# Kernel optimization log

Hardware: AMD Instinct MI355X
Metric: run time of the kernel (lower is better)

## Reference

```python
import jax, jax.numpy as jnp
import numpy as np

LN_EPS = 1e-9

def _layer_norm(x, g, b):
    mu = jnp.mean(x, axis=-1, keepdims=True)
    var = jnp.mean((x - mu) ** 2, axis=-1, keepdims=True)
    return (x - mu) * jax.lax.rsqrt(var + LN_EPS) * g + b

def _ffn(x, w1, b1, w2, b2, ln_g, ln_b):
    h = jax.nn.gelu(x @ w1 + b1, approximate=False)
    h = h @ w2 + b2
    return _layer_norm(h, ln_g, ln_b)

def _kernel_mean(x, y):
    d = x.shape[1]
    x2 = jnp.sum(x * x, axis=1)[:, None]
    y2 = jnp.sum(y * y, axis=1)[None, :]
    sq = x2 + y2 - 2.0 * (x @ y.T)  # [Nx, Ny]
    return jnp.mean(jnp.exp(-sq / (d * d)))

def _mmd(x, y):
    return _kernel_mean(x, x) + _kernel_mean(y, y) - 2.0 * _kernel_mean(x, y)

def setup_inputs() -> dict:
    key = jax.random.key(0)
    ks = jax.random.split(key, 8)
    B, S, D, DI, DL = 8, 512, 1024, 4096, 64
    s = lambda fan: 1.0 / np.sqrt(fan)
    return {
        "hidden": jax.random.normal(ks[0], (B, S, D), jnp.float32),
        "true_samples": jax.random.normal(ks[1], (B * S, DL), jnp.float32),
        "enc_w1": jax.random.normal(ks[2], (D, DI), jnp.float32) * s(D),
        "enc_b1": jnp.zeros((DI,), jnp.float32),
        "enc_w2": jax.random.normal(ks[3], (DI, DL), jnp.float32) * s(DI),
        "enc_b2": jnp.zeros((DL,), jnp.float32),
        "enc_ln_g": jnp.ones((DL,), jnp.float32),
        "enc_ln_b": jnp.zeros((DL,), jnp.float32),
        "dec_w1": jax.random.normal(ks[4], (DL, DI), jnp.float32) * s(DL),
        "dec_b1": jnp.zeros((DI,), jnp.float32),
        "dec_w2": jax.random.normal(ks[5], (DI, D), jnp.float32) * s(DI),
        "dec_b2": jnp.zeros((D,), jnp.float32),
        "dec_ln_g": jnp.ones((D,), jnp.float32),
        "dec_ln_b": jnp.zeros((D,), jnp.float32),
    }

def reference(hidden, true_samples, enc_w1, enc_b1, enc_w2, enc_b2, enc_ln_g, enc_ln_b,
              dec_w1, dec_b1, dec_w2, dec_b2, dec_ln_g, dec_ln_b):
    latent = _ffn(hidden, enc_w1, enc_b1, enc_w2, enc_b2, enc_ln_g, enc_ln_b)  # [B,S,DL]
    recon = _ffn(latent, dec_w1, dec_b1, dec_w2, dec_b2, dec_ln_g, dec_ln_b)   # [B,S,D]
    B, S, DL = latent.shape
    lat_flat = latent.reshape(-1, DL)  # [B*S, DL]
    reg_loss = _mmd(true_samples, lat_flat) / B * S
    return recon, latent, reg_loss
```

## Files before the change

### kernel.cpp

```cpp
#include <hip/hip_runtime.h>
#include <hip/hip_bf16.h>
#include <math.h>


typedef __attribute__((ext_vector_type(8))) short short8;
typedef __attribute__((ext_vector_type(4))) float float4a;
typedef __attribute__((ext_vector_type(4))) unsigned short us4;

__device__ inline ushort bf16r(float x) {
    union { float f; unsigned u; } c; c.f = x;
    unsigned r = (c.u + 0x7fffu + ((c.u >> 16) & 1u)) >> 16;
    return (ushort)r;
}

__device__ inline void gld_lds16(const void* g, void* l) {
    __builtin_amdgcn_global_load_lds(
        (const __attribute__((address_space(1))) void*)g,
        (__attribute__((address_space(3))) void*)l, 16, 0, 0);
}

template <int N> __device__ inline void wait_vmcnt() {
    if constexpr (N == 0) asm volatile("s_waitcnt vmcnt(0)" ::: "memory");
    else if constexpr (N == 4) asm volatile("s_waitcnt vmcnt(4)" ::: "memory");
    else if constexpr (N == 6) asm volatile("s_waitcnt vmcnt(6)" ::: "memory");
}

template <int N> __device__ inline void wait_lgkmcnt() {
    if constexpr (N == 0) asm volatile("s_waitcnt lgkmcnt(0)" ::: "memory");
    else if constexpr (N == 2) asm volatile("s_waitcnt lgkmcnt(2)" ::: "memory");
    else if constexpr (N == 4) asm volatile("s_waitcnt lgkmcnt(4)" ::: "memory");
    else if constexpr (N == 6) asm volatile("s_waitcnt lgkmcnt(6)" ::: "memory");
    else if constexpr (N == 8) asm volatile("s_waitcnt lgkmcnt(8)" ::: "memory");
    else if constexpr (N == 12) asm volatile("s_waitcnt lgkmcnt(12)" ::: "memory");
}

__device__ inline float fast_gelu(float v) {
    float v2 = v * v;
    float u = v * __builtin_fmaf(0.07135481627f, v2, 1.5957691216f);
    u = fminf(u, 30.0f);
    float e = __expf(u);
    return v * e * __builtin_amdgcn_rcpf(e + 1.0f);
}

__global__ __launch_bounds__(256) void k_pre(
        const float* __restrict__ hidden, ushort* __restrict__ A1bf,
        const float* __restrict__ tsamp, ushort* __restrict__ Tbf,
        float* __restrict__ sq_t, float* __restrict__ acc,
        const float* __restrict__ i0, ushort* __restrict__ o0,
        const float* __restrict__ i1, ushort* __restrict__ o1,
        const float* __restrict__ i2, ushort* __restrict__ o2,
        const float* __restrict__ i3, ushort* __restrict__ o3) {
    int b = blockIdx.x, tid = threadIdx.x;
    if (b == 0 && tid < 24) acc[tid] = 0.0f;
    if (b < 4096) {
        int i = b * 1024 + tid * 4;
        float4 v = *(const float4*)(hidden + i);
        us4 o = {bf16r(v.x), bf16r(v.y), bf16r(v.z), bf16r(v.w)};
        *(us4*)(A1bf + i) = o;
        return;
    }
    if (b < 4352) {
        int i = (b - 4096) * 1024 + tid * 4;
        float4 v = *(const float4*)(tsamp + i);
        us4 o = {bf16r(v.x), bf16r(v.y), bf16r(v.z), bf16r(v.w)};
        *(us4*)(Tbf + i) = o;
        float s = v.x * v.x + v.y * v.y + v.z * v.z + v.w * v.w;
#pragma unroll
        for (int off = 8; off; off >>= 1) s += __shfl_xor(s, off);
        if ((tid & 15) == 0) sq_t[i >> 6] = s;
        return;
    }
    __shared__ float t[32][65];
    const float* in; ushort* out; int R, C;
    int lb = b - 4352;
    if (lb < 2048)      { in = i0; out = o0; R = 1024; C = 4096; }
    else if (lb < 2176) { in = i1; out = o1; R = 4096; C = 64;   lb -= 2048; }
    else if (lb < 2304) { in = i2; out = o2; R = 64;   C = 4096; lb -= 2176; }
    else                { in = i3; out = o3; R = 4096; C = 1024; lb -= 2304; }
    int bx = (lb % (C / 32)) * 32;
    int by = (lb / (C / 32)) * 64;
    int tx = tid & 31, ty = tid >> 5;
#pragma unroll
    for (int i = 0; i < 64; i += 8)
        t[tx][i + ty] = in[(size_t)(by + i + ty) * C + (bx + tx)];
    __syncthreads();
#pragma unroll
    for (int i = 0; i < 32; i += 8) {
        int c = i + ty;
        ushort2 o;
        o.x = bf16r(t[c][2 * tx]);
        o.y = bf16r(t[c][2 * tx + 1]);
        *(ushort2*)(&out[(size_t)(bx + c) * R + by + 2 * tx]) = o;
    }
}

template <int BN, int EPI, bool SWZ>
__global__ __launch_bounds__(256) void k_gemm(
        const ushort* __restrict__ A, const ushort* __restrict__ Bt,
        const float* __restrict__ bias, void* __restrict__ Out,
        float* __restrict__ Out2, int M, int N, int K, int KC) {
    constexpr int BM = 128, BK = 64;
    constexpr int WAVES_N = BN / 64;
    constexpr int WAVES_M = 4 / WAVES_N;
    constexpr int WM = BM / WAVES_M;
    constexpr int MT = WM / 16;
    constexpr int NT = 4;
    constexpr int CA = BM / 32, CB = BN / 32;

    __shared__ ushort sA[BM * 64];
    __shared__ ushort sB[BN * 64];

    const int tid  = threadIdx.x;
    const int wave = tid >> 6, lane = tid & 63;
    const int wm = wave / WAVES_N, wn = wave % WAVES_N;
    int bx = blockIdx.x, by = blockIdx.y;
    if constexpr (SWZ) {
        int lin = blockIdx.x + gridDim.x * blockIdx.y;
        by = lin % gridDim.y;
        bx = lin / gridDim.y;
    }
    const int m0 = by * BM, n0 = bx * BN;
    const int lrow = lane & 15, lq = lane >> 4;
    const int srow8 = lane >> 3;
    const int sk8   = lane & 7;
    const int kbeg = blockIdx.z * KC;

    const ushort* pA[CA]; unsigned lA[CA];
#pragma unroll
    for (int j = 0; j < CA; ++j) {
        int c = wave * CA + j;
        int r = c * 8 + srow8;
        pA[j] = &A[(size_t)(m0 + r) * K + kbeg + ((sk8 ^ (r & 7)) * 8)];
        lA[j] = c * 512;
    }
    const ushort* pB[CB]; unsigned lB[CB];
#pragma unroll
    for (int j = 0; j < CB; ++j) {
        int c = wave * CB + j;
        int r = c * 8 + srow8;
        pB[j] = &Bt[(size_t)(n0 + r) * K + kbeg + ((sk8 ^ (r & 7)) * 8)];
        lB[j] = c * 512;
    }
    unsigned aoff[2][MT], boff[2][NT];
#pragma unroll
    for (int h = 0; h < 2; ++h) {
#pragma unroll
        for (int mt = 0; mt < MT; ++mt) {
            int r = wm * WM + mt * 16 + lrow;
            aoff[h][mt] = r * 64 + (((h * 4 + lq) ^ (r & 7)) * 8);
        }
#pragma unroll
        for (int nt = 0; nt < NT; ++nt) {
            int r = wn * 64 + nt * 16 + lrow;
            boff[h][nt] = r * 64 + (((h * 4 + lq) ^ (r & 7)) * 8);
        }
    }

    float4a acc[MT][NT];
#pragma unroll
    for (int mt = 0; mt < MT; ++mt)
#pragma unroll
        for (int nt = 0; nt < NT; ++nt)
            acc[mt][nt] = (float4a){0.f, 0.f, 0.f, 0.f};

    for (int k0 = 0; k0 < KC; k0 += BK) {
#pragma unroll
        for (int j = 0; j < CA; ++j) {
            gld_lds16(pA[j], &sA[lA[j]]);
            pA[j] += BK;
        }
#pragma unroll
        for (int j = 0; j < CB; ++j) {
            gld_lds16(pB[j], &sB[lB[j]]);
            pB[j] += BK;
        }
        __syncthreads();
#pragma unroll
        for (int h = 0; h < 2; ++h) {
            short8 af[MT], bfr[NT];
#pragma unroll
            for (int mt = 0; mt < MT; ++mt)
                af[mt] = *(short8*)(&sA[aoff[h][mt]]);
#pragma unroll
            for (int nt = 0; nt < NT; ++nt)
                bfr[nt] = *(short8*)(&sB[boff[h][nt]]);
#pragma unroll
            for (int mt = 0; mt < MT; ++mt)
#pragma unroll
                for (int nt = 0; nt < NT; ++nt)
                    acc[mt][nt] = __builtin_amdgcn_mfma_f32_16x16x32_bf16(
                        af[mt], bfr[nt], acc[mt][nt], 0, 0, 0);
        }
        __syncthreads();
    }

    float* dstp = nullptr;
    if constexpr (EPI == 2) {
        if (Out2 && blockIdx.z) dstp = Out2;
        else dstp = (float*)Out + (size_t)blockIdx.z * M * N;
    }
#pragma unroll
    for (int mt = 0; mt < MT; ++mt)
#pragma unroll
        for (int nt = 0; nt < NT; ++nt) {
            int col = n0 + wn * 64 + nt * 16 + lrow;
            float bv = 0.f;
            if constexpr (EPI != 2) bv = bias[col];
#pragma unroll
            for (int r = 0; r < 4; ++r) {
                int row = m0 + wm * WM + mt * 16 + lq * 4 + r;
                float v = acc[mt][nt][r] + bv;
                if constexpr (EPI == 0) {
                    ((ushort*)Out)[(size_t)row * N + col] = bf16r(fast_gelu(v));
                } else if constexpr (EPI == 1) {
                    ((float*)Out)[(size_t)row * N + col] = v;
                } else {
                    dstp[(size_t)row * N + col] = v;
                }
            }
        }
}

template <int BN, int EPI, int CX, int CY>
__global__ __launch_bounds__(512, 2) void k_gemm256mb(
        const ushort* __restrict__ A, const ushort* __restrict__ Bt,
        const float* __restrict__ bias, void* __restrict__ Out,
        float* __restrict__ Out2, int M, int N, int K, int KC) {
    constexpr int BM = 256, BK = 64;
    constexpr int AI = 4;
    constexpr int BI = BN / 64;
    constexpr int WAVES_N = BN / 64;
    constexpr int WAVES_M = 8 / WAVES_N;
    constexpr int WM = BM / WAVES_M;
    constexpr int MT = WM / 16;
    constexpr int NT = 4;

    __shared__ ushort sA[2][BM * 64];
    __shared__ ushort sB[2][BN * 64];

    const int tid = threadIdx.x;
    const int wave = tid >> 6, lane = tid & 63;
    const int wm = wave / WAVES_N, wn = wave % WAVES_N;

    const int gx = gridDim.x, gy = gridDim.y;
    const int lin = blockIdx.x + gx * (blockIdx.y + gy * blockIdx.z);
    const int nwg = gx * gy * gridDim.z;
    const int cpx = nwg >> 3;
    const int swz = (lin & 7) * cpx + (lin >> 3);
    const int nz  = gx * gy;
    const int zz  = swz / nz;
    const int rr  = swz % nz;
    const int chunk = rr / (CX * CY);
    const int lcl   = rr % (CX * CY);
    const int ncx   = gx / CX;
    const int bx = (chunk % ncx) * CX + (lcl % CX);
    const int by = (chunk / ncx) * CY + (lcl / CX);

    const int m0 = by * BM, n0 = bx * BN;
    const int lrow = lane & 15, lq = lane >> 4;
    const int kbeg = zz * KC;
    const int nT = KC / BK;

    const int crow = tid >> 3;
    const int ck8  = (tid & 7) ^ (crow & 7);
    const ushort* pAbase = A  + (size_t)(m0 + crow) * K + kbeg + ck8 * 8;
    const ushort* pBbase = Bt + (size_t)(n0 + crow) * K + kbeg + ck8 * 8;

    const int a0  = (wm * WM + lrow) * 64;
    const int b0  = (wn * 64 + lrow) * 64;
    const int sw0 = ((lq) ^ (lrow & 7)) * 8;
    const int sw1 = ((4 + lq) ^ (lrow & 7)) * 8;

    float4a acc[MT][NT];
#pragma unroll
    for (int mt = 0; mt < MT; ++mt)
#pragma unroll
        for (int nt = 0; nt < NT; ++nt)
            acc[mt][nt] = (float4a){0.f, 0.f, 0.f, 0.f};

#pragma unroll
    for (int j = 0; j < AI; ++j)
        gld_lds16(pAbase + (size_t)j * 64 * K, &sA[0][j * 4096 + wave * 512]);
#pragma unroll
    for (int j = 0; j < BI; ++j)
        gld_lds16(pBbase + (size_t)j * 64 * K, &sB[0][j * 4096 + wave * 512]);
    wait_vmcnt<0>();
    __builtin_amdgcn_s_barrier();
    __builtin_amdgcn_sched_barrier(0);

    for (int t = 0; t < nT; ++t) {
        const int d = t & 1;
        const bool pf1 = (t + 1 < nT);
        const size_t koff1 = (size_t)(t + 1) * BK;

        short8 af0[MT], bfr0[NT], af1[MT], bfr1[NT];
#pragma unroll
        for (int mt = 0; mt < MT; ++mt)
            af0[mt] = *(const short8*)(&sA[d][a0 + mt * 1024 + sw0]);
#pragma unroll
        for (int nt = 0; nt < NT; ++nt)
            bfr0[nt] = *(const short8*)(&sB[d][b0 + nt * 1024 + sw0]);
        __builtin_amdgcn_sched_barrier(0);
#pragma unroll
        for (int mt = 0; mt < MT; ++mt)
            af1[mt] = *(const short8*)(&sA[d][a0 + mt * 1024 + sw1]);
#pragma unroll
        for (int nt = 0; nt < NT; ++nt)
            bfr1[nt] = *(const short8*)(&sB[d][b0 + nt * 1024 + sw1]);
        if (pf1) {
#pragma unroll
            for (int j = 0; j < AI; ++j)
                gld_lds16(pAbase + (size_t)j * 64 * K + koff1,
                          &sA[d ^ 1][j * 4096 + wave * 512]);
#pragma unroll
            for (int j = 0; j < BI; ++j)
                gld_lds16(pBbase + (size_t)j * 64 * K + koff1,
                          &sB[d ^ 1][j * 4096 + wave * 512]);
        }
        wait_lgkmcnt<MT + 4>();
        __builtin_amdgcn_sched_barrier(0);
        __builtin_amdgcn_s_setprio(1);
#pragma unroll
        for (int mt = 0; mt < MT; ++mt)
#pragma unroll
            for (int nt = 0; nt < NT; ++nt)
                acc[mt][nt] = __builtin_amdgcn_mfma_f32_16x16x32_bf16(
                    af0[mt], bfr0[nt], acc[mt][nt], 0, 0, 0);
        __builtin_amdgcn_s_setprio(0);
        wait_lgkmcnt<0>();
        __builtin_amdgcn_sched_barrier(0);
        __builtin_amdgcn_s_setprio(1);
#pragma unroll
        for (int mt = 0; mt < MT; ++mt)
#pragma unroll
            for (int nt = 0; nt < NT; ++nt)
                acc[mt][nt] = __builtin_amdgcn_mfma_f32_16x16x32_bf16(
                    af1[mt], bfr1[nt], acc[mt][nt], 0, 0, 0);
        __builtin_amdgcn_s_setprio(0);
        if (pf1) {
            wait_vmcnt<0>();
            __builtin_amdgcn_s_barrier();
            __builtin_amdgcn_sched_barrier(0);
        }
    }

    float* dstp = nullptr;
    if constexpr (EPI == 2) {
        if (Out2 && zz) dstp = Out2;
        else dstp = (float*)Out + (size_t)zz * M * N;
    }
#pragma unroll
    for (int mt = 0; mt < MT; ++mt)
#pragma unroll
        for (int nt = 0; nt < NT; ++nt) {
            const int col = n0 + wn * 64 + nt * 16 + lrow;
            float bv = 0.f;
            if constexpr (EPI == 0) bv = bias[col];
#pragma unroll
            for (int r = 0; r < 4; ++r) {
                const int row = m0 + wm * WM + mt * 16 + lq * 4 + r;
                float v = acc[mt][nt][r] + bv;
                if constexpr (EPI == 0)
                    ((ushort*)Out)[(size_t)row * N + col] = bf16r(fast_gelu(v));
                else
                    dstp[(size_t)row * N + col] = v;
            }
        }
}

__global__ __launch_bounds__(512, 2) void k_gemm1f(
        const ushort* __restrict__ A, const ushort* __restrict__ Bt,
        const float* __restrict__ bias, const ushort* __restrict__ W2t,
        float* __restrict__ part, int M, int N, int K) {
    constexpr int BM = 256, BN = 256, BK = 64;
    constexpr int AI = 4, BI = 4;
    constexpr int WAVES_N = 4;
    constexpr int WM = 128;
    constexpr int MT = 8, NT = 4;
    constexpr int CX = 4, CY = 8;

    __shared__ ushort smem[65536];

    const int tid = threadIdx.x;
    const int wave = tid >> 6, lane = tid & 63;
    const int wm = wave / WAVES_N, wn = wave % WAVES_N;

    const int gx = gridDim.x, gy = gridDim.y;
    const int lin = blockIdx.x + gx * blockIdx.y;
    const int cpx = (gx * gy) >> 3;
    const int swz = (lin & 7) * cpx + (lin >> 3);
    const int chunk = swz / (CX * CY);
    const int lcl   = swz % (CX * CY);
    const int ncx   = gx / CX;
    const int bx = (chunk % ncx) * CX + (lcl % CX);
    const int by = (chunk / ncx) * CY + (lcl / CX);

    const int m0 = by * BM, n0 = bx * BN;
    const int lrow = lane & 15, lq = lane >> 4;
    const int nT = K / BK;

    const int crow = tid >> 3;
    const int ck8  = (tid & 7) ^ (crow & 7);
    const ushort* pAbase = A  + (size_t)(m0 + crow) * K + ck8 * 8;
    const ushort* pBbase = Bt + (size_t)(n0 + crow) * K + ck8 * 8;

    const int a0  = (wm * WM + lrow) * 64;
    const int b0  = (wn * 64 + lrow) * 64;
    const int sw0 = ((lq) ^ (lrow & 7)) * 8;
    const int sw1 = ((4 + lq) ^ (lrow & 7)) * 8;

    float4a acc[MT][NT];
#pragma unroll
    for (int mt = 0; mt < MT; ++mt)
#pragma unroll
        for (int nt = 0; nt < NT; ++nt)
            acc[mt][nt] = (float4a){0.f, 0.f, 0.f, 0.f};

#pragma unroll
    for (int j = 0; j < AI; ++j)
        gld_lds16(pAbase + (size_t)j * 64 * K, &smem[j * 4096 + wave * 512]);
#pragma unroll
    for (int j = 0; j < BI; ++j)
        gld_lds16(pBbase + (size_t)j * 64 * K,
                  &smem[32768 + j * 4096 + wave * 512]);
    wait_vmcnt<0>();
    __builtin_amdgcn_s_barrier();
    __builtin_amdgcn_sched_barrier(0);

    for (int t = 0; t < nT; ++t) {
        const int d = t & 1;
        const bool pf1 = (t + 1 < nT);
        const size_t koff1 = (size_t)(t + 1) * BK;
        const ushort* sAd = &smem[d * 16384];
        const ushort* sBd = &smem[32768 + d * 16384];

        short8 af0[MT], bfr0[NT], af1[MT], bfr1[NT];
#pragma unroll
        for (int mt = 0; mt < MT; ++mt)
            af0[mt] = *(const short8*)(&sAd[a0 + mt * 1024 + sw0]);
#pragma unroll
        for (int nt = 0; nt < NT; ++nt)
            bfr0[nt] = *(const short8*)(&sBd[b0 + nt * 1024 + sw0]);
        __builtin_amdgcn_sched_barrier(0);
#pragma unroll
        for (int mt = 0; mt < MT; ++mt)
            af1[mt] = *(const short8*)(&sAd[a0 + mt * 1024 + sw1]);
#pragma unroll
        for (int nt = 0; nt < NT; ++nt)
            bfr1[nt] = *(const short8*)(&sBd[b0 + nt * 1024 + sw1]);
        if (pf1) {
#pragma unroll
            for (int j = 0; j < AI; ++j)
                gld_lds16(pAbase + (size_t)j * 64 * K + koff1,
                          &smem[(d ^ 1) * 16384 + j * 4096 + wave * 512]);
#pragma unroll
            for (int j = 0; j < BI; ++j)
                gld_lds16(pBbase + (size_t)j * 64 * K + koff1,
                          &smem[32768 + (d ^ 1) * 16384 + j * 4096 + wave * 512]);
        }
        wait_lgkmcnt<12>();
        __builtin_amdgcn_sched_barrier(0);
        __builtin_amdgcn_s_setprio(1);
#pragma unroll
        for (int mt = 0; mt < MT; ++mt)
#pragma unroll
            for (int nt = 0; nt < NT; ++nt)
                acc[mt][nt] = __builtin_amdgcn_mfma_f32_16x16x32_bf16(
                    af0[mt], bfr0[nt], acc[mt][nt], 0, 0, 0);
        __builtin_amdgcn_s_setprio(0);
        wait_lgkmcnt<0>();
        __builtin_amdgcn_sched_barrier(0);
        __builtin_amdgcn_s_setprio(1);
#pragma unroll
        for (int mt = 0; mt < MT; ++mt)
#pragma unroll
            for (int nt = 0; nt < NT; ++nt)
                acc[mt][nt] = __builtin_amdgcn_mfma_f32_16x16x32_bf16(
                    af1[mt], bfr1[nt], acc[mt][nt], 0, 0, 0);
        __builtin_amdgcn_s_setprio(0);
        if (pf1) {
            wait_vmcnt<0>();
            __builtin_amdgcn_s_barrier();
            __builtin_amdgcn_sched_barrier(0);
        }
    }

    __syncthreads();
#pragma unroll
    for (int mt = 0; mt < MT; ++mt)
#pragma unroll
        for (int nt = 0; nt < NT; ++nt) {
            const int c = wn * 64 + nt * 16 + lrow;
            const float bv = bias[n0 + c];
            const int s = c >> 3, cl = c & 7;
#pragma unroll
            for (int r_ = 0; r_ < 4; ++r_) {
                const int r = wm * WM + mt * 16 + lq * 4 + r_;
                const int sz = (s & 24) | ((s & 7) ^ (r & 7));
                smem[r * 256 + sz * 8 + cl] =
                    bf16r(fast_gelu(acc[mt][nt][r_] + bv));
            }
        }
    __syncthreads();

    float4a pacc[2][4];
#pragma unroll
    for (int m2 = 0; m2 < 2; ++m2)
#pragma unroll
        for (int n2 = 0; n2 < 4; ++n2)
            pacc[m2][n2] = (float4a){0.f, 0.f, 0.f, 0.f};

    const ushort* gW2 = W2t + n0;
#pragma unroll
    for (int kk = 0; kk < 8; ++kk) {
        short8 af2[2], bf2[4];
#pragma unroll
        for (int m2 = 0; m2 < 2; ++m2) {
            const int r2 = wave * 32 + m2 * 16 + lrow;
            const int s2 = kk * 4 + lq;
            const int sz2 = (s2 & 24) | ((s2 & 7) ^ (r2 & 7));
            af2[m2] = *(const short8*)(&smem[r2 * 256 + sz2 * 8]);
        }
#pragma unroll
        for (int n2 = 0; n2 < 4; ++n2) {
            const int l = n2 * 16 + lrow;
            bf2[n2] = *(const short8*)(&gW2[(size_t)l * 4096 + kk * 32 + lq * 8]);
        }
#pragma unroll
        for (int m2 = 0; m2 < 2; ++m2)
#pragma unroll
            for (int n2 = 0; n2 < 4; ++n2)
                pacc[m2][n2] = __builtin_amdgcn_mfma_f32_16x16x32_bf16(
                    af2[m2], bf2[n2], pacc[m2][n2], 0, 0, 0);
    }

    float* pz = part + (size_t)bx * M * 64;
#pragma unroll
    for (int m2 = 0; m2 < 2; ++m2)
#pragma unroll
        for (int n2 = 0; n2 < 4; ++n2) {
            const int lat = n2 * 16 + lrow;
#pragma unroll
            for (int r_ = 0; r_ < 4; ++r_) {
                const int row = m0 + wave * 32 + m2 * 16 + lq * 4 + r_;
                pz[(size_t)row * 64 + lat] = pacc[m2][n2][r_];
            }
        }
}

__global__ __launch_bounds__(256) void k_gram_all(
        const ushort* __restrict__ Tbf, const ushort* __restrict__ Lbf,
        const float* __restrict__ sq_t, const float* __restrict__ sq_l,
        float* __restrict__ accum) {
    __shared__ ushort sX[128 * 64];
    __shared__ ushort sY[128 * 64];
    __shared__ float red[4];

    int id = blockIdx.x;
    int pair, tbx, tby; float w;
    if (id < 1056) {
        pair = (id < 528) ? 0 : 1;
        int t = (pair == 0) ? id : id - 528;
        int r = (int)((sqrtf(8.0f * t + 1.0f) - 1.0f) * 0.5f);
        while ((r + 1) * (r + 2) / 2 <= t) ++r;
        while (r * (r + 1) / 2 > t) --r;
        tby = r; tbx = t - r * (r + 1) / 2;
        w = (tbx == tby) ? 1.0f : 2.0f;
    } else {
        pair = 2; int t = id - 1056;
        tbx = t & 31; tby = t >> 5; w = 1.0f;
    }
    const ushort* Xb = (pair == 1) ? Lbf : Tbf;
    const ushort* Yb = (pair == 0) ? Tbf : Lbf;
    const float* sqX = (pair == 1) ? sq_l : sq_t;
    const float* sqY = (pair == 0) ? sq_t : sq_l;

    const int tid  = threadIdx.x;
    const int wave = tid >> 6, lane = tid & 63;
    const int wm = wave >> 1, wn = wave & 1;
    const int bx = tbx * 128, by = tby * 128;
    const int lrow = lane & 15, lq = lane >> 4;
    const int srow8 = lane >> 3, sk8 = lane & 7;

#pragma unroll
    for (int j = 0; j < 4; ++j) {
        int c = wave * 4 + j;
        int r = c * 8 + srow8;
        int kc = (sk8 ^ (r & 7)) * 8;
        gld_lds16(&Xb[(size_t)(bx + r) * 64 + kc], &sX[c * 512]);
        gld_lds16(&Yb[(size_t)(by + r) * 64 + kc], &sY[c * 512]);
    }

    unsigned xoff[2][4], yoff[2][4];
#pragma unroll
    for (int h = 0; h < 2; ++h)
#pragma unroll
        for (int i = 0; i < 4; ++i) {
            int rx = wm * 64 + i * 16 + lrow;
            int ry = wn * 64 + i * 16 + lrow;
            xoff[h][i] = rx * 64 + (((h * 4 + lq) ^ (rx & 7)) * 8);
            yoff[h][i] = ry * 64 + (((h * 4 + lq) ^ (ry & 7)) * 8);
        }
    __syncthreads();

    float4a acc[4][4];
#pragma unroll
    for (int mt = 0; mt < 4; ++mt)
#pragma unroll
        for (int nt = 0; nt < 4; ++nt)
            acc[mt][nt] = (float4a){0.f, 0.f, 0.f, 0.f};

#pragma unroll
    for (int h = 0; h < 2; ++h) {
        short8 xf[4], yf[4];
#pragma unroll
        for (int mt = 0; mt < 4; ++mt)
            xf[mt] = *(short8*)(&sX[xoff[h][mt]]);
#pragma unroll
        for (int nt = 0; nt < 4; ++nt)
            yf[nt] = *(short8*)(&sY[yoff[h][nt]]);
#pragma unroll
        for (int mt = 0; mt < 4; ++mt)
#pragma unroll
            for (int nt = 0; nt < 4; ++nt)
                acc[mt][nt] = __builtin_amdgcn_mfma_f32_16x16x32_bf16(
                    xf[mt], yf[nt], acc[mt][nt], 0, 0, 0);
    }

    float sy[4];
#pragma unroll
    for (int nt = 0; nt < 4; ++nt)
        sy[nt] = sqY[by + wn * 64 + nt * 16 + lrow];
    float s = 0.f;
#pragma unroll
    for (int mt = 0; mt < 4; ++mt)
#pragma unroll
        for (int r = 0; r < 4; ++r) {
            float sx = sqX[bx + wm * 64 + mt * 16 + lq * 4 + r];
#pragma unroll
            for (int nt = 0; nt < 4; ++nt)
                s += __expf((2.0f * acc[mt][nt][r] - sx - sy[nt]) * (1.0f / 4096.0f));
        }
    s *= w;
#pragma unroll
    for (int off = 32; off; off >>= 1) s += __shfl_xor(s, off);
    if ((tid & 63) == 0) red[tid >> 6] = s;
    __syncthreads();
    if (tid == 0) atomicAdd(accum + pair * 8, red[0] + red[1] + red[2] + red[3]);
}

__global__ __launch_bounds__(256) void k_ln64_red(
        const float* __restrict__ part, int npart,
        const float* __restrict__ bias, const float* __restrict__ g,
        const float* __restrict__ b, float* __restrict__ outf,
        ushort* __restrict__ outb, float* __restrict__ sq_l) {
    int wave = threadIdx.x >> 6, lane = threadIdx.x & 63;
    int row = blockIdx.x * 4 + wave;
    float x = bias[lane];
    for (int s = 0; s < npart; ++s)
        x += part[(size_t)s * 4096 * 64 + row * 64 + lane];
    float s = x;
#pragma unroll
    for (int off = 32; off; off >>= 1) s += __shfl_xor(s, off);
    float mu = s * (1.0f / 64.0f);
    float d = x - mu;
    float v = d * d;
#pragma unroll
    for (int off = 32; off; off >>= 1) v += __shfl_xor(v, off);
    float rs = rsqrtf(v * (1.0f / 64.0f) + 1e-9f);
    float y = d * rs * g[lane] + b[lane];
    outf[row * 64 + lane] = y;
    outb[row * 64 + lane] = bf16r(y);
    float q = y * y;
#pragma unroll
    for (int off = 32; off; off >>= 1) q += __shfl_xor(q, off);
    if (lane == 0) sq_l[row] = q;
}

__global__ __launch_bounds__(256) void k_ln1024_red(
        const float* __restrict__ p0, const float* __restrict__ p1,
        const float* __restrict__ bias, const float* __restrict__ g,
        const float* __restrict__ b, float* __restrict__ out) {
    __shared__ float red[4];
    int row = blockIdx.x, tid = threadIdx.x;
    const float4 v0 = *(const float4*)(p0 + (size_t)row * 1024 + tid * 4);
    const float4 v1 = *(const float4*)(p1 + (size_t)row * 1024 + tid * 4);
    const float4 bb = *(const float4*)(bias + tid * 4);
    float4 v;
    v.x = v0.x + v1.x + bb.x;
    v.y = v0.y + v1.y + bb.y;
    v.z = v0.z + v1.z + bb.z;
    v.w = v0.w + v1.w + bb.w;
    float s = v.x + v.y + v.z + v.w;
#pragma unroll
    for (int off = 32; off; off >>= 1) s += __shfl_xor(s, off);
    if ((tid & 63) == 0) red[tid >> 6] = s;
    __syncthreads();
    float mu = (red[0] + red[1] + red[2] + red[3]) * (1.0f / 1024.0f);
    float dx = v.x - mu, dy = v.y - mu, dz = v.z - mu, dw = v.w - mu;
    float q = dx * dx + dy * dy + dz * dz + dw * dw;
#pragma unroll
    for (int off = 32; off; off >>= 1) q += __shfl_xor(q, off);
    __syncthreads();
    if ((tid & 63) == 0) red[tid >> 6] = q;
    __syncthreads();
    float rs = rsqrtf((red[0] + red[1] + red[2] + red[3]) * (1.0f / 1024.0f) + 1e-9f);
    const float4 gv = *(const float4*)(g + tid * 4);
    const float4 bv = *(const float4*)(b + tid * 4);
    float4 o;
    o.x = dx * rs * gv.x + bv.x;
    o.y = dy * rs * gv.y + bv.y;
    o.z = dz * rs * gv.z + bv.z;
    o.w = dw * rs * gv.w + bv.w;
    *(float4*)(out + (size_t)row * 1024 + tid * 4) = o;
}

__global__ void k_finalize(const float* __restrict__ accum, float* __restrict__ out) {
    out[0] = (accum[0] + accum[8] - 2.0f * accum[16]) * (64.0f / (4096.0f * 4096.0f));
}

extern "C" void kernel_launch(void* const* d_in, const int* in_sizes, int n_in,
                              void* d_out, int out_size, void* d_ws, size_t ws_size,
                              hipStream_t stream) {
    const float* hidden   = (const float*)d_in[0];
    const float* tsamp    = (const float*)d_in[1];
    const float* enc_w1   = (const float*)d_in[2];
    const float* enc_b1   = (const float*)d_in[3];
    const float* enc_w2   = (const float*)d_in[4];
    const float* enc_b2   = (const float*)d_in[5];
    const float* enc_ln_g = (const float*)d_in[6];
    const float* enc_ln_b = (const float*)d_in[7];
    const float* dec_w1   = (const float*)d_in[8];
    const float* dec_b1   = (const float*)d_in[9];
    const float* dec_w2   = (const float*)d_in[10];
    const float* dec_b2   = (const float*)d_in[11];
    const float* dec_ln_g = (const float*)d_in[12];
    const float* dec_ln_b = (const float*)d_in[13];

    float* out      = (float*)d_out;
    float* recon    = out;
    float* latent_f = out + 4194304;
    float* reg      = out + 4456448;

    char* ws = (char*)d_ws;
    const size_t MB = 1024 * 1024;
    ushort* A1bf = (ushort*)(ws + 0);
    ushort* W1t  = (ushort*)(ws + 8 * MB);
    float*  h4p0 = (float*)(ws + 0);
    ushort* H1bf = (ushort*)(ws + 16 * MB);
    float*  part = (float*)(ws + 16 * MB);
    ushort* W4t  = (ushort*)(ws + 48 * MB);
    ushort* W2t  = (ushort*)(ws + 56 * MB);
    ushort* W3t  = (ushort*)(ws + 56 * MB + 512 * 1024);
    ushort* Lbf  = (ushort*)(ws + 57 * MB);
    float*  sq_t = (float*)(ws + 59 * MB);
    float*  sq_l = (float*)(ws + 59 * MB + 16384);
    float*  acc3 = (float*)(ws + 59 * MB + 32768);
    ushort* Tbf  = (ushort*)(ws + 59 * MB + 65536);

    k_pre<<<8704, 256, 0, stream>>>(hidden, A1bf, tsamp, Tbf, sq_t, acc3,
                                    enc_w1, W1t, enc_w2, W2t,
                                    dec_w1, W3t, dec_w2, W4t);

    k_gemm1f<<<dim3(16, 16, 1), 512, 0, stream>>>(
        A1bf, W1t, enc_b1, W2t, part, 4096, 4096, 1024);
    k_ln64_red<<<1024, 256, 0, stream>>>(part, 16, enc_b2, enc_ln_g, enc_ln_b,
                                         latent_f, Lbf, sq_l);

    k_gemm<64, 0, false><<<dim3(64, 32, 1), 256, 0, stream>>>(
        Lbf, W3t, dec_b1, H1bf, nullptr, 4096, 4096, 64, 64);
    k_gemm256mb<128, 2, 8, 4><<<dim3(8, 16, 2), 512, 0, stream>>>(
        H1bf, W4t, nullptr, h4p0, recon, 4096, 1024, 4096, 2048);
    k_ln1024_red<<<4096, 256, 0, stream>>>(h4p0, recon, dec_b2, dec_ln_g,
                                           dec_ln_b, recon);

    k_gram_all<<<2080, 256, 0, stream>>>(Tbf, Lbf, sq_t, sq_l, acc3);
    k_finalize<<<1, 1, 0, stream>>>(acc3, reg);
}
```

Measured before the change: 260.6 us.

## Triple-buffer decoder GEMM, fold MMD finalize into gram kernel, reorder launches

```diff
diff --git a/kernel.cpp b/kernel.cpp
--- a/kernel.cpp
+++ b/kernel.cpp
@@ -27,9 +27,6 @@
 
 template <int N> __device__ inline void wait_lgkmcnt() {
     if constexpr (N == 0) asm volatile("s_waitcnt lgkmcnt(0)" ::: "memory");
-    else if constexpr (N == 2) asm volatile("s_waitcnt lgkmcnt(2)" ::: "memory");
-    else if constexpr (N == 4) asm volatile("s_waitcnt lgkmcnt(4)" ::: "memory");
-    else if constexpr (N == 6) asm volatile("s_waitcnt lgkmcnt(6)" ::: "memory");
     else if constexpr (N == 8) asm volatile("s_waitcnt lgkmcnt(8)" ::: "memory");
     else if constexpr (N == 12) asm volatile("s_waitcnt lgkmcnt(12)" ::: "memory");
 }
@@ -51,7 +48,7 @@
         const float* __restrict__ i2, ushort* __restrict__ o2,
         const float* __restrict__ i3, ushort* __restrict__ o3) {
     int b = blockIdx.x, tid = threadIdx.x;
-    if (b == 0 && tid < 24) acc[tid] = 0.0f;
+    if (b == 0 && tid < 32) acc[tid] = 0.0f;
     if (b < 4096) {
         int i = b * 1024 + tid * 4;
         float4 v = *(const float4*)(hidden + i);
@@ -221,22 +218,18 @@
         }
 }
 
-template <int BN, int EPI, int CX, int CY>
-__global__ __launch_bounds__(512, 2) void k_gemm256mb(
+template <int CX, int CY>
+__global__ __launch_bounds__(512, 2) void k_gemm4p3(
         const ushort* __restrict__ A, const ushort* __restrict__ Bt,
-        const float* __restrict__ bias, void* __restrict__ Out,
-        float* __restrict__ Out2, int M, int N, int K, int KC) {
-    constexpr int BM = 256, BK = 64;
-    constexpr int AI = 4;
-    constexpr int BI = BN / 64;
-    constexpr int WAVES_N = BN / 64;
-    constexpr int WAVES_M = 8 / WAVES_N;
-    constexpr int WM = BM / WAVES_M;
-    constexpr int MT = WM / 16;
-    constexpr int NT = 4;
-
-    __shared__ ushort sA[2][BM * 64];
-    __shared__ ushort sB[2][BN * 64];
+        void* __restrict__ Out, float* __restrict__ Out2,
+        int M, int N, int K, int KC) {
+    constexpr int BM = 256, BN = 128, BK = 64;
+    constexpr int AI = 4, BI = 2;
+    constexpr int WAVES_N = 2;
+    constexpr int WM = 64, MT = 4, NT = 4;
+
+    __shared__ ushort sA[3][BM * 64];
+    __shared__ ushort sB[3][BN * 64];
 
     const int tid = threadIdx.x;
     const int wave = tid >> 6, lane = tid & 63;
@@ -284,14 +277,27 @@
 #pragma unroll
     for (int j = 0; j < BI; ++j)
         gld_lds16(pBbase + (size_t)j * 64 * K, &sB[0][j * 4096 + wave * 512]);
-    wait_vmcnt<0>();
+    if (nT > 1) {
+#pragma unroll
+        for (int j = 0; j < AI; ++j)
+            gld_lds16(pAbase + (size_t)j * 64 * K + BK,
+                      &sA[1][j * 4096 + wave * 512]);
+#pragma unroll
+        for (int j = 0; j < BI; ++j)
+            gld_lds16(pBbase + (size_t)j * 64 * K + BK,
+                      &sB[1][j * 4096 + wave * 512]);
+        wait_vmcnt<6>();
+    } else {
+        wait_vmcnt<0>();
+    }
     __builtin_amdgcn_s_barrier();
     __builtin_amdgcn_sched_barrier(0);
 
     for (int t = 0; t < nT; ++t) {
-        const int d = t & 1;
-        const bool pf1 = (t + 1 < nT);
-        const size_t koff1 = (size_t)(t + 1) * BK;
+        const int d  = t % 3;
+        const int dn = (t + 2) % 3;
+        const bool pf1 = (t + 1 < nT), pf2 = (t + 2 < nT);
+        const size_t koff2 = (size_t)(t + 2) * BK;
 
         short8 af0[MT], bfr0[NT], af1[MT], bfr1[NT];
 #pragma unroll
@@ -307,17 +313,17 @@
 #pragma unroll
         for (int nt = 0; nt < NT; ++nt)
             bfr1[nt] = *(const short8*)(&sB[d][b0 + nt * 1024 + sw1]);
-        if (pf1) {
+        if (pf2) {
 #pragma unroll
             for (int j = 0; j < AI; ++j)
-                gld_lds16(pAbase + (size_t)j * 64 * K + koff1,
-                          &sA[d ^ 1][j * 4096 + wave * 512]);
+                gld_lds16(pAbase + (size_t)j * 64 * K + koff2,
+                          &sA[dn][j * 4096 + wave * 512]);
 #pragma unroll
             for (int j = 0; j < BI; ++j)
-                gld_lds16(pBbase + (size_t)j * 64 * K + koff1,
-                          &sB[d ^ 1][j * 4096 + wave * 512]);
-        }
-        wait_lgkmcnt<MT + 4>();
+                gld_lds16(pBbase + (size_t)j * 64 * K + koff2,
+                          &sB[dn][j * 4096 + wave * 512]);
+        }
+        wait_lgkmcnt<8>();
         __builtin_amdgcn_sched_barrier(0);
         __builtin_amdgcn_s_setprio(1);
 #pragma unroll
@@ -337,33 +343,29 @@
                 acc[mt][nt] = __builtin_amdgcn_mfma_f32_16x16x32_bf16(
                     af1[mt], bfr1[nt], acc[mt][nt], 0, 0, 0);
         __builtin_amdgcn_s_setprio(0);
-        if (pf1) {
+        if (pf2) {
+            wait_vmcnt<6>();
+            __builtin_amdgcn_s_barrier();
+            __builtin_amdgcn_sched_barrier(0);
+        } else if (pf1) {
             wait_vmcnt<0>();
             __builtin_amdgcn_s_barrier();
             __builtin_amdgcn_sched_barrier(0);
         }
     }
 
-    float* dstp = nullptr;
-    if constexpr (EPI == 2) {
-        if (Out2 && zz) dstp = Out2;
-        else dstp = (float*)Out + (size_t)zz * M * N;
-    }
+    float* dstp;
+    if (Out2 && zz) dstp = Out2;
+    else dstp = (float*)Out + (size_t)zz * M * N;
 #pragma unroll
     for (int mt = 0; mt < MT; ++mt)
 #pragma unroll
         for (int nt = 0; nt < NT; ++nt) {
             const int col = n0 + wn * 64 + nt * 16 + lrow;
-            float bv = 0.f;
-            if constexpr (EPI == 0) bv = bias[col];
 #pragma unroll
             for (int r = 0; r < 4; ++r) {
                 const int row = m0 + wm * WM + mt * 16 + lq * 4 + r;
-                float v = acc[mt][nt][r] + bv;
-                if constexpr (EPI == 0)
-                    ((ushort*)Out)[(size_t)row * N + col] = bf16r(fast_gelu(v));
-                else
-                    dstp[(size_t)row * N + col] = v;
+                dstp[(size_t)row * N + col] = acc[mt][nt][r];
             }
         }
 }
@@ -430,7 +432,7 @@
     for (int t = 0; t < nT; ++t) {
         const int d = t & 1;
         const bool pf1 = (t + 1 < nT);
-        const size_t koff1 = (size_t)(t + 1) * BK;
+        const size_t koff1 = (size_t)(t + 1) * 64;
         const ushort* sAd = &smem[d * 16384];
         const ushort* sBd = &smem[32768 + d * 16384];
 
@@ -551,7 +553,7 @@
 __global__ __launch_bounds__(256) void k_gram_all(
         const ushort* __restrict__ Tbf, const ushort* __restrict__ Lbf,
         const float* __restrict__ sq_t, const float* __restrict__ sq_l,
-        float* __restrict__ accum) {
+        float* __restrict__ accum, float* __restrict__ regout) {
     __shared__ ushort sX[128 * 64];
     __shared__ ushort sY[128 * 64];
     __shared__ float red[4];
@@ -646,7 +648,17 @@
     for (int off = 32; off; off >>= 1) s += __shfl_xor(s, off);
     if ((tid & 63) == 0) red[tid >> 6] = s;
     __syncthreads();
-    if (tid == 0) atomicAdd(accum + pair * 8, red[0] + red[1] + red[2] + red[3]);
+    if (tid == 0) {
+        atomicAdd(accum + pair * 8, red[0] + red[1] + red[2] + red[3]);
+        __threadfence();
+        unsigned prev = atomicAdd((unsigned*)(accum + 24), 1u);
+        if (prev == 2079) {
+            float a0 = atomicAdd(accum + 0, 0.0f);
+            float a1 = atomicAdd(accum + 8, 0.0f);
+            float a2 = atomicAdd(accum + 16, 0.0f);
+            regout[0] = (a0 + a1 - 2.0f * a2) * (64.0f / (4096.0f * 4096.0f));
+        }
+    }
 }
 
 __global__ __launch_bounds__(256) void k_ln64_red(
@@ -713,10 +725,6 @@
     o.z = dz * rs * gv.z + bv.z;
     o.w = dw * rs * gv.w + bv.w;
     *(float4*)(out + (size_t)row * 1024 + tid * 4) = o;
-}
-
-__global__ void k_finalize(const float* __restrict__ accum, float* __restrict__ out) {
-    out[0] = (accum[0] + accum[8] - 2.0f * accum[16]) * (64.0f / (4096.0f * 4096.0f));
 }
 
 extern "C" void kernel_launch(void* const* d_in, const int* in_sizes, int n_in,
@@ -767,13 +775,12 @@
     k_ln64_red<<<1024, 256, 0, stream>>>(part, 16, enc_b2, enc_ln_g, enc_ln_b,
                                          latent_f, Lbf, sq_l);
 
+    k_gram_all<<<2080, 256, 0, stream>>>(Tbf, Lbf, sq_t, sq_l, acc3, reg);
+
     k_gemm<64, 0, false><<<dim3(64, 32, 1), 256, 0, stream>>>(
         Lbf, W3t, dec_b1, H1bf, nullptr, 4096, 4096, 64, 64);
-    k_gemm256mb<128, 2, 8, 4><<<dim3(8, 16, 2), 512, 0, stream>>>(
-        H1bf, W4t, nullptr, h4p0, recon, 4096, 1024, 4096, 2048);
+    k_gemm4p3<8, 4><<<dim3(8, 16, 2), 512, 0, stream>>>(
+        H1bf, W4t, h4p0, recon, 4096, 1024, 4096, 2048);
     k_ln1024_red<<<4096, 256, 0, stream>>>(h4p0, recon, dec_b2, dec_ln_g,
                                            dec_ln_b, recon);
-
-    k_gram_all<<<2080, 256, 0, stream>>>(Tbf, Lbf, sq_t, sq_l, acc3);
-    k_finalize<<<1, 1, 0, stream>>>(acc3, reg);
-}
+}
```

Result: slower. 282.7 us (+8.5%).
